# Optimization experiments

Hardware: AMD Instinct MI355X
Metric: run time of the kernel (lower is better)

## Reference

```python
import jax, jax.numpy as jnp
import numpy as np

N_NODES = 100000
N_EDGES = 1600000
C = 64          # in = hidden = out channels
L = 3           # num_layers
BN_EPS = 1e-5


def setup_inputs() -> dict:
    key = jax.random.key(0)
    ks = jax.random.split(key, 16)
    x = jax.random.normal(ks[0], (N_NODES, C), dtype=jnp.float32)
    edge_index = jax.random.randint(ks[1], (2, N_EDGES), 0, N_NODES, dtype=jnp.int32)
    s = 1.0 / np.sqrt(C)
    # Stacked per-layer parameters (all layers are C->C).
    # Linear weights stored as [in, out] (i.e. torch weight transposed).
    W1 = jax.random.normal(ks[2], (L, C, C), dtype=jnp.float32) * s
    b1 = jnp.zeros((L, C), dtype=jnp.float32)
    g1 = jnp.ones((L, C), dtype=jnp.float32)    # MLP BN1 gamma
    be1 = jnp.zeros((L, C), dtype=jnp.float32)  # MLP BN1 beta
    W2 = jax.random.normal(ks[3], (L, C, C), dtype=jnp.float32) * s
    b2 = jnp.zeros((L, C), dtype=jnp.float32)
    g2 = jnp.ones((L, C), dtype=jnp.float32)
    be2 = jnp.zeros((L, C), dtype=jnp.float32)
    bn_g = jnp.ones((L, C), dtype=jnp.float32)   # outer per-layer BN gamma
    bn_be = jnp.zeros((L, C), dtype=jnp.float32)
    eps = jnp.zeros((L,), dtype=jnp.float32)     # GIN eps per layer
    return {"x": x, "edge_index": edge_index, "eps": eps,
            "W1": W1, "b1": b1, "g1": g1, "be1": be1,
            "W2": W2, "b2": b2, "g2": g2, "be2": be2,
            "bn_g": bn_g, "bn_be": bn_be}


def _bn(h, g, b):
    # Inference-mode BatchNorm1d with running_mean=0, running_var=1.
    return g * (h * (1.0 / np.sqrt(1.0 + BN_EPS))) + b


def reference(x, edge_index, eps, W1, b1, g1, be1, W2, b2, g2, be2, bn_g, bn_be):
    src, dst = edge_index[0], edge_index[1]
    for i in range(L):
        # GIN message passing: gather source features, scatter-add to targets.
        agg = jax.ops.segment_sum(x[src], dst, num_segments=N_NODES)  # [N, C]
        h = (1.0 + eps[i]) * x + agg
        # 2-layer MLP: Linear -> BN -> ReLU, twice.
        h = jax.nn.relu(_bn(h @ W1[i] + b1[i], g1[i], be1[i]))
        h = jax.nn.relu(_bn(h @ W2[i] + b2[i], g2[i], be2[i]))
        # Outer per-layer BatchNorm.
        x = _bn(h, bn_g[i], bn_be[i])
        if i < L - 1:
            x = jax.nn.relu(x)  # dropout is identity in eval mode
    return x
```

## Files before the change

### kernel.cpp

```cpp
#include <hip/hip_runtime.h>
#include <hip/hip_fp16.h>

#define N_NODES 100000
#define N_EDGES 1600000
#define CH 64
#define NLAYERS 3
#define NBUCKC 98
#define SLABC 18432
#define SUBCAP 2304
#define EPB 8192

typedef _Float16 half8 __attribute__((ext_vector_type(8)));
typedef float floatx4 __attribute__((ext_vector_type(4)));

static __device__ __forceinline__ float4 ld4(const float* p){ return *(const float4*)p; }
static __device__ __forceinline__ unsigned pack2(float a, float b){
  __half2 h = __float22half2_rn(make_float2(a, b));
  return *(unsigned*)&h;
}
static __device__ __forceinline__ float2 up2(unsigned u){
  __half2 h = *(__half2*)&u;
  return __half22float2(h);
}

__global__ __launch_bounds__(256) void binit_kernel(int* __restrict__ btail){
  int i = blockIdx.x*256 + threadIdx.x;
  if (i < NBUCKC) btail[i] = i*SLABC;
}

__global__ __launch_bounds__(256) void part_kernel(const int* __restrict__ src, const int* __restrict__ dst,
                                                   int* __restrict__ btail, int* __restrict__ pairs){
  __shared__ int lpos[NBUCKC];
  __shared__ int gb[NBUCKC];
  int tid = threadIdx.x;
  if (tid < NBUCKC) lpos[tid] = 0;
  __syncthreads();
  int base = blockIdx.x * EPB;
  #pragma unroll 4
  for (int k = 0; k < EPB/256; ++k) {
    int e = base + k*256 + tid;
    if (e < N_EDGES) atomicAdd(&lpos[dst[e] >> 10], 1);
  }
  __syncthreads();
  if (tid < NBUCKC) {
    int cc = lpos[tid];
    gb[tid] = cc ? atomicAdd(&btail[tid], cc) : 0;
    lpos[tid] = 0;
  }
  __syncthreads();
  #pragma unroll 4
  for (int k = 0; k < EPB/256; ++k) {
    int e = base + k*256 + tid;
    if (e < N_EDGES) {
      int d = dst[e];
      int bk = d >> 10;
      int p = atomicAdd(&lpos[bk], 1);
      int idx = gb[bk] + p;
      if (idx < (bk+1)*SLABC)
        pairs[idx] = src[e] | ((d & 1023) << 20);
    }
  }
}

__global__ __launch_bounds__(256) void csr_kernel(const int* __restrict__ pairs, const int* __restrict__ btail,
                                                  int* __restrict__ offs, int* __restrict__ offe,
                                                  int* __restrict__ srclist){
  __shared__ int c[128];
  __shared__ int s[128];
  __shared__ int cur[128];
  int t = threadIdx.x;
  int b = blockIdx.x >> 3;
  int j = blockIdx.x & 7;
  int e0 = b*SLABC;
  int e1 = btail[b]; int emax = e0 + SLABC; if (e1 > emax) e1 = emax;
  if (t < 128) c[t] = 0;
  __syncthreads();
  for (int i = e0 + t; i < e1; i += 256) {
    int p = pairs[i];
    int dl = (unsigned)p >> 20;
    if ((dl >> 7) == j) atomicAdd(&c[dl & 127], 1);
  }
  __syncthreads();
  int v = (t < 128) ? c[t] : 0;
  if (t < 128) s[t] = v;
  __syncthreads();
  #pragma unroll
  for (int o = 1; o < 128; o <<= 1){
    int u = 0;
    if (t < 128 && t >= o) u = s[t-o];
    __syncthreads();
    if (t < 128) s[t] += u;
    __syncthreads();
  }
  int base = e0 + j*SUBCAP;
  if (t < 128) {
    int excl = s[t] - v;
    cur[t] = excl;
    int n = b*1024 + j*128 + t;
    if (n < N_NODES) { offs[n] = base + excl; offe[n] = base + excl + v; }
  }
  __syncthreads();
  for (int i = e0 + t; i < e1; i += 256) {
    int p = pairs[i];
    int dl = (unsigned)p >> 20;
    if ((dl >> 7) == j) {
      int pos = atomicAdd(&cur[dl & 127], 1);
      if (pos < SUBCAP)
        srclist[base + pos] = p & 0xFFFFF;
    }
  }
}

__global__ __launch_bounds__(256) void prep_kernel(
    const float* __restrict__ W1, const float* __restrict__ b1,
    const float* __restrict__ g1, const float* __restrict__ be1,
    const float* __restrict__ W2, const float* __restrict__ b2,
    const float* __restrict__ g2, const float* __restrict__ be2,
    const float* __restrict__ bng, const float* __restrict__ bnb,
    _Float16* __restrict__ Wt, float* __restrict__ bf, float* __restrict__ ogb){
  const float s = 0.9999950000374997f;
  int i = blockIdx.x*256 + threadIdx.x;
  if (i < NLAYERS*4096) {
    int l = i >> 12, rem = i & 4095, k = rem >> 6, n = rem & 63;
    int di = n*64 + (((k>>3) ^ (n&7))<<3) + (k&7);
    Wt[l*8192 + di]        = (_Float16)(W1[i] * g1[l*64+n] * s);
    Wt[l*8192 + 4096 + di] = (_Float16)(W2[i] * g2[l*64+n] * s);
  }
  if (i < NLAYERS*64) {
    int l = i >> 6, j = i & 63;
    bf[l*128 + j]      = b1[i]*g1[i]*s + be1[i];
    bf[l*128 + 64 + j] = b2[i]*g2[i]*s + be2[i];
    ogb[i]                 = bng[i]*s;
    ogb[NLAYERS*64 + i]    = bnb[i];
  }
}

__global__ __launch_bounds__(256) void xcvt_kernel(const float* __restrict__ x, unsigned short* __restrict__ xb){
  int i = (blockIdx.x*256 + threadIdx.x)*8;
  if (i < N_NODES*CH) {
    float4 v0 = ld4(x + i), v1 = ld4(x + i + 4);
    uint4 w;
    w.x = pack2(v0.x, v0.y); w.y = pack2(v0.z, v0.w);
    w.z = pack2(v1.x, v1.y); w.w = pack2(v1.z, v1.w);
    *(uint4*)(xb + i) = w;
  }
}

__global__ __launch_bounds__(256) void layer_kernel(const unsigned short* __restrict__ XBin,
                                                    const int* __restrict__ offs, const int* __restrict__ offe,
                                                    const int* __restrict__ srclist,
                                                    const float* __restrict__ eps,
                                                    const _Float16* __restrict__ Wt,
                                                    const float* __restrict__ bf, const float* __restrict__ ogb,
                                                    int layer, float* __restrict__ outf,
                                                    _Float16* __restrict__ outb, int relu_out){
  __shared__ _Float16 HsA[64*64];
  __shared__ _Float16 Wts[64*64];
  int tid = threadIdx.x;
  int b = blockIdx.x;
  const _Float16* Wg = Wt + layer*8192;
  *(uint4*)&Wts[tid*8]       = *(const uint4*)&Wg[tid*8];
  *(uint4*)&Wts[(tid+256)*8] = *(const uint4*)&Wg[(tid+256)*8];

  float ep = 1.0f + eps[layer];
  int kb = tid & 7;
  const unsigned short* xr = XBin + (kb << 3);
  #pragma unroll
  for (int p = 0; p < 2; ++p) {
    int nl = p*32 + (tid >> 3);
    int n = b*64 + nl;
    float A[8] = {0,0,0,0,0,0,0,0};
    float B[8] = {0,0,0,0,0,0,0,0};
    float C[8] = {0,0,0,0,0,0,0,0};
    float D[8] = {0,0,0,0,0,0,0,0};
    float r[8] = {0,0,0,0,0,0,0,0};
    if (n < N_NODES) {
      #define ADD8(acc, u) { float2 f; \
        f = up2((u).x); acc[0] += f.x; acc[1] += f.y; \
        f = up2((u).y); acc[2] += f.x; acc[3] += f.y; \
        f = up2((u).z); acc[4] += f.x; acc[5] += f.y; \
        f = up2((u).w); acc[6] += f.x; acc[7] += f.y; }
      int e0 = offs[n], e1 = offe[n];
      int e = e0;
      for (; e+4 <= e1; e += 4) {
        int s0 = srclist[e], s1 = srclist[e+1], s2 = srclist[e+2], s3 = srclist[e+3];
        uint4 u0 = *(const uint4*)(xr + (size_t)s0*CH);
        uint4 u1 = *(const uint4*)(xr + (size_t)s1*CH);
        uint4 u2 = *(const uint4*)(xr + (size_t)s2*CH);
        uint4 u3 = *(const uint4*)(xr + (size_t)s3*CH);
        ADD8(A, u0) ADD8(B, u1) ADD8(C, u2) ADD8(D, u3)
      }
      for (; e < e1; ++e) {
        int s0 = srclist[e];
        uint4 u0 = *(const uint4*)(xr + (size_t)s0*CH);
        ADD8(A, u0)
      }
      #undef ADD8
      uint4 sv = *(const uint4*)(xr + (size_t)n*CH);
      float sf[8];
      { float2 f;
        f = up2(sv.x); sf[0]=f.x; sf[1]=f.y;
        f = up2(sv.y); sf[2]=f.x; sf[3]=f.y;
        f = up2(sv.z); sf[4]=f.x; sf[5]=f.y;
        f = up2(sv.w); sf[6]=f.x; sf[7]=f.y; }
      #pragma unroll
      for (int i = 0; i < 8; ++i) r[i] = fmaf(ep, sf[i], (A[i] + B[i]) + (C[i] + D[i]));
    }
    uint4 w;
    w.x = pack2(r[0], r[1]); w.y = pack2(r[2], r[3]);
    w.z = pack2(r[4], r[5]); w.w = pack2(r[6], r[7]);
    *(uint4*)&HsA[nl*64 + ((kb ^ (nl&7))<<3)] = w;
  }
  __syncthreads();

  int lane = tid & 63;
  int wid = tid >> 6;
  int c = lane & 15;
  int q = lane >> 4;
  int mbase = wid*16;
  int ma = mbase + c;

  half8 a0 = *(const half8*)&HsA[ma*64 + (((q)   ^ (ma&7))<<3)];
  half8 a1 = *(const half8*)&HsA[ma*64 + (((4+q) ^ (ma&7))<<3)];

  floatx4 acc[4];
  #pragma unroll
  for (int nt = 0; nt < 4; ++nt) {
    int n = nt*16 + c;
    float bv = bf[layer*128 + n];
    floatx4 Acc = {bv, bv, bv, bv};
    half8 b0 = *(const half8*)&Wts[n*64 + (((q)   ^ (n&7))<<3)];
    half8 b1 = *(const half8*)&Wts[n*64 + (((4+q) ^ (n&7))<<3)];
    Acc = __builtin_amdgcn_mfma_f32_16x16x32_f16(a0, b0, Acc, 0, 0, 0);
    Acc = __builtin_amdgcn_mfma_f32_16x16x32_f16(a1, b1, Acc, 0, 0, 0);
    acc[nt] = Acc;
  }
  __syncthreads();

  #pragma unroll
  for (int nt = 0; nt < 4; ++nt) {
    int n = nt*16 + c;
    #pragma unroll
    for (int r = 0; r < 4; ++r) {
      int m = mbase + q*4 + r;
      float h = acc[nt][r]; h = h > 0.f ? h : 0.f;
      HsA[m*64 + (((n>>3) ^ (m&7))<<3) + (n&7)] = (_Float16)h;
    }
  }
  *(uint4*)&Wts[tid*8]       = *(const uint4*)&Wg[4096 + tid*8];
  *(uint4*)&Wts[(tid+256)*8] = *(const uint4*)&Wg[4096 + (tid+256)*8];
  __syncthreads();

  half8 c0 = *(const half8*)&HsA[ma*64 + (((q)   ^ (ma&7))<<3)];
  half8 c1 = *(const half8*)&HsA[ma*64 + (((4+q) ^ (ma&7))<<3)];
  floatx4 acc2[4];
  #pragma unroll
  for (int nt = 0; nt < 4; ++nt) {
    int n = nt*16 + c;
    float bv = bf[layer*128 + 64 + n];
    floatx4 Acc = {bv, bv, bv, bv};
    half8 b0 = *(const half8*)&Wts[n*64 + (((q)   ^ (n&7))<<3)];
    half8 b1 = *(const half8*)&Wts[n*64 + (((4+q) ^ (n&7))<<3)];
    Acc = __builtin_amdgcn_mfma_f32_16x16x32_f16(c0, b0, Acc, 0, 0, 0);
    Acc = __builtin_amdgcn_mfma_f32_16x16x32_f16(c1, b1, Acc, 0, 0, 0);
    acc2[nt] = Acc;
  }

  #pragma unroll
  for (int nt = 0; nt < 4; ++nt) {
    int n = nt*16 + c;
    float og = ogb[layer*64 + n];
    float ob = ogb[NLAYERS*64 + layer*64 + n];
    #pragma unroll
    for (int r = 0; r < 4; ++r) {
      int m = mbase + q*4 + r;
      int gnode = b*64 + m;
      if (gnode < N_NODES) {
        float h = acc2[nt][r]; h = h > 0.f ? h : 0.f;
        float o = fmaf(og, h, ob);
        if (relu_out) {
          o = o > 0.f ? o : 0.f;
          outb[(size_t)gnode*CH + n] = (_Float16)o;
        } else {
          outf[(size_t)gnode*CH + n] = o;
        }
      }
    }
  }
}

extern "C" void kernel_launch(void* const* d_in, const int* in_sizes, int n_in,
                              void* d_out, int out_size, void* d_ws, size_t ws_size,
                              hipStream_t stream) {
  const float* x0  = (const float*)d_in[0];
  const int*   ei  = (const int*)d_in[1];
  const float* eps = (const float*)d_in[2];
  const float* W1  = (const float*)d_in[3];
  const float* b1  = (const float*)d_in[4];
  const float* g1  = (const float*)d_in[5];
  const float* be1 = (const float*)d_in[6];
  const float* W2  = (const float*)d_in[7];
  const float* b2  = (const float*)d_in[8];
  const float* g2  = (const float*)d_in[9];
  const float* be2 = (const float*)d_in[10];
  const float* bng = (const float*)d_in[11];
  const float* bnb = (const float*)d_in[12];
  const int* src = ei;
  const int* dst = ei + N_EDGES;
  float* OUT = (float*)d_out;

  char* p = (char*)d_ws;
  auto carve = [&](size_t bytes)->char*{ char* r = p; p += (bytes + 255) & ~(size_t)255; return r; };
  int*   offs    = (int*)carve((size_t)N_NODES*sizeof(int));
  int*   offe    = (int*)carve((size_t)N_NODES*sizeof(int));
  int*   btail   = (int*)carve(NBUCKC*sizeof(int));
  int*   pairs   = (int*)carve((size_t)NBUCKC*SLABC*sizeof(int));
  int*   srclist = (int*)carve((size_t)NBUCKC*SLABC*sizeof(int));
  unsigned short* XB0 = (unsigned short*)carve((size_t)N_NODES*CH*2);
  unsigned short* XB1 = (unsigned short*)carve((size_t)N_NODES*CH*2);
  _Float16* Wt   = (_Float16*)carve((size_t)NLAYERS*2*4096*2);
  float* bfb     = (float*)carve((size_t)NLAYERS*2*64*sizeof(float));
  float* ogb     = (float*)carve((size_t)2*NLAYERS*64*sizeof(float));

  const int npart = (N_EDGES + EPB - 1)/EPB;
  binit_kernel<<<1, 256, 0, stream>>>(btail);
  part_kernel<<<npart, 256, 0, stream>>>(src, dst, btail, pairs);
  csr_kernel<<<NBUCKC*8, 256, 0, stream>>>(pairs, btail, offs, offe, srclist);
  prep_kernel<<<48, 256, 0, stream>>>(W1,b1,g1,be1,W2,b2,g2,be2,bng,bnb,Wt,bfb,ogb);
  xcvt_kernel<<<(N_NODES*CH/8 + 255)/256, 256, 0, stream>>>(x0, XB0);

  const int nlb = (N_NODES + 63)/64;
  layer_kernel<<<nlb, 256, 0, stream>>>(XB0, offs, offe, srclist, eps, Wt, bfb, ogb, 0, OUT, (_Float16*)XB1, 1);
  layer_kernel<<<nlb, 256, 0, stream>>>(XB1, offs, offe, srclist, eps, Wt, bfb, ogb, 1, OUT, (_Float16*)XB0, 1);
  layer_kernel<<<nlb, 256, 0, stream>>>(XB0, offs, offe, srclist, eps, Wt, bfb, ogb, 2, OUT, (_Float16*)XB1, 0);
}
```

Baseline: 322.2 us.

## Add second-level fine bucket partition before CSR build

```diff
diff --git a/kernel.cpp b/kernel.cpp
--- a/kernel.cpp
+++ b/kernel.cpp
@@ -7,7 +7,8 @@
 #define NLAYERS 3
 #define NBUCKC 98
 #define SLABC 18432
-#define SUBCAP 2304
+#define NFINE (NBUCKC*8)
+#define SLABF 2560
 #define EPB 8192
 
 typedef _Float16 half8 __attribute__((ext_vector_type(8)));
@@ -23,13 +24,14 @@
   return __half22float2(h);
 }
 
-__global__ __launch_bounds__(256) void binit_kernel(int* __restrict__ btail){
+__global__ __launch_bounds__(256) void binit_kernel(int* __restrict__ btail, int* __restrict__ ftail){
   int i = blockIdx.x*256 + threadIdx.x;
   if (i < NBUCKC) btail[i] = i*SLABC;
-}
-
-__global__ __launch_bounds__(256) void part_kernel(const int* __restrict__ src, const int* __restrict__ dst,
-                                                   int* __restrict__ btail, int* __restrict__ pairs){
+  if (i < NFINE)  ftail[i] = i*SLABF;
+}
+
+__global__ __launch_bounds__(256) void part1_kernel(const int* __restrict__ src, const int* __restrict__ dst,
+                                                    int* __restrict__ btail, int* __restrict__ pairs){
   __shared__ int lpos[NBUCKC];
   __shared__ int gb[NBUCKC];
   int tid = threadIdx.x;
@@ -62,23 +64,79 @@
   }
 }
 
-__global__ __launch_bounds__(256) void csr_kernel(const int* __restrict__ pairs, const int* __restrict__ btail,
+__global__ __launch_bounds__(256) void part2_kernel(const int* __restrict__ pairs, const int* __restrict__ btail,
+                                                    int* __restrict__ ftail, int* __restrict__ pairs2){
+  __shared__ int cnt[8*32];
+  __shared__ int scur[8];
+  int tid = threadIdx.x;
+  int b = blockIdx.x >> 3;
+  int sg = blockIdx.x & 7;
+  int e0 = b*SLABC;
+  int e1 = btail[b]; int emax = e0 + SLABC; if (e1 > emax) e1 = emax;
+  int len = e1 - e0;
+  int s0 = e0 + (int)(((long)len * sg) >> 3);
+  int s1 = e0 + (int)(((long)len * (sg+1)) >> 3);
+  if (tid < 256) { cnt[tid & 255] = 0; }
+  __syncthreads();
+  for (int i = s0 + tid; i < s1; i += 256) {
+    int p = pairs[i];
+    int fk = ((unsigned)p >> 27);
+    atomicAdd(&cnt[(fk<<5) + (tid & 31)], 1);
+  }
+  __syncthreads();
+  if (tid < 8) {
+    int tot = 0;
+    #pragma unroll
+    for (int r = 0; r < 32; ++r) tot += cnt[(tid<<5) + r];
+    scur[tid] = tot ? atomicAdd(&ftail[(b<<3) + tid], tot) : 0;
+  }
+  __syncthreads();
+  int lane = tid & 63;
+  int wbase = s0 + (tid >> 6)*64;
+  for (int i = wbase; i < s1; i += 256) {
+    int idx = i + lane - (tid >> 6)*64 + (tid >> 6)*64;
+    int e = i + lane - lane + lane;
+    (void)idx; (void)e;
+    int ei = i + lane - lane;
+    int my = ei + lane;
+    bool valid = (my < s1);
+    int p = valid ? pairs[my] : 0;
+    int fk = valid ? (int)((unsigned)p >> 27) : -1;
+    #pragma unroll
+    for (int j = 0; j < 8; ++j) {
+      unsigned long long mask = __ballot(valid && fk == j);
+      if (mask) {
+        int leader = __ffsll((long long)mask) - 1;
+        int cc = __popcll(mask);
+        int basep = 0;
+        if (lane == leader) basep = atomicAdd(&scur[j], cc);
+        basep = __shfl(basep, leader, 64);
+        if (valid && fk == j) {
+          int rank = __popcll(mask & ((1ull << lane) - 1ull));
+          int pos = basep + rank;
+          if (pos < ((b<<3) + j + 1)*SLABF)
+            pairs2[pos] = p;
+        }
+      }
+    }
+  }
+}
+
+__global__ __launch_bounds__(256) void csr_kernel(const int* __restrict__ pairs2, const int* __restrict__ ftail,
                                                   int* __restrict__ offs, int* __restrict__ offe,
                                                   int* __restrict__ srclist){
   __shared__ int c[128];
   __shared__ int s[128];
   __shared__ int cur[128];
   int t = threadIdx.x;
-  int b = blockIdx.x >> 3;
-  int j = blockIdx.x & 7;
-  int e0 = b*SLABC;
-  int e1 = btail[b]; int emax = e0 + SLABC; if (e1 > emax) e1 = emax;
+  int f = blockIdx.x;
+  int e0 = f*SLABF;
+  int e1 = ftail[f]; int emax = e0 + SLABF; if (e1 > emax) e1 = emax;
   if (t < 128) c[t] = 0;
   __syncthreads();
   for (int i = e0 + t; i < e1; i += 256) {
-    int p = pairs[i];
-    int dl = (unsigned)p >> 20;
-    if ((dl >> 7) == j) atomicAdd(&c[dl & 127], 1);
+    int p = pairs2[i];
+    atomicAdd(&c[((unsigned)p >> 20) & 127], 1);
   }
   __syncthreads();
   int v = (t < 128) ? c[t] : 0;
@@ -92,22 +150,18 @@
     if (t < 128) s[t] += u;
     __syncthreads();
   }
-  int base = e0 + j*SUBCAP;
   if (t < 128) {
     int excl = s[t] - v;
     cur[t] = excl;
-    int n = b*1024 + j*128 + t;
-    if (n < N_NODES) { offs[n] = base + excl; offe[n] = base + excl + v; }
+    int n = (f >> 3)*1024 + (f & 7)*128 + t;
+    if (n < N_NODES) { offs[n] = e0 + excl; offe[n] = e0 + excl + v; }
   }
   __syncthreads();
   for (int i = e0 + t; i < e1; i += 256) {
-    int p = pairs[i];
-    int dl = (unsigned)p >> 20;
-    if ((dl >> 7) == j) {
-      int pos = atomicAdd(&cur[dl & 127], 1);
-      if (pos < SUBCAP)
-        srclist[base + pos] = p & 0xFFFFF;
-    }
+    int p = pairs2[i];
+    int pos = atomicAdd(&cur[((unsigned)p >> 20) & 127], 1);
+    if (pos < SLABF)
+      srclist[e0 + pos] = p & 0xFFFFF;
   }
 }
 
@@ -314,8 +368,10 @@
   int*   offs    = (int*)carve((size_t)N_NODES*sizeof(int));
   int*   offe    = (int*)carve((size_t)N_NODES*sizeof(int));
   int*   btail   = (int*)carve(NBUCKC*sizeof(int));
+  int*   ftail   = (int*)carve(NFINE*sizeof(int));
   int*   pairs   = (int*)carve((size_t)NBUCKC*SLABC*sizeof(int));
-  int*   srclist = (int*)carve((size_t)NBUCKC*SLABC*sizeof(int));
+  int*   pairs2  = (int*)carve((size_t)NFINE*SLABF*sizeof(int));
+  int*   srclist = (int*)carve((size_t)NFINE*SLABF*sizeof(int));
   unsigned short* XB0 = (unsigned short*)carve((size_t)N_NODES*CH*2);
   unsigned short* XB1 = (unsigned short*)carve((size_t)N_NODES*CH*2);
   _Float16* Wt   = (_Float16*)carve((size_t)NLAYERS*2*4096*2);
@@ -323,9 +379,10 @@
   float* ogb     = (float*)carve((size_t)2*NLAYERS*64*sizeof(float));
 
   const int npart = (N_EDGES + EPB - 1)/EPB;
-  binit_kernel<<<1, 256, 0, stream>>>(btail);
-  part_kernel<<<npart, 256, 0, stream>>>(src, dst, btail, pairs);
-  csr_kernel<<<NBUCKC*8, 256, 0, stream>>>(pairs, btail, offs, offe, srclist);
+  binit_kernel<<<(NFINE+255)/256, 256, 0, stream>>>(btail, ftail);
+  part1_kernel<<<npart, 256, 0, stream>>>(src, dst, btail, pairs);
+  part2_kernel<<<NFINE, 256, 0, stream>>>(pairs, btail, ftail, pairs2);
+  csr_kernel<<<NFINE, 256, 0, stream>>>(pairs2, ftail, offs, offe, srclist);
   prep_kernel<<<48, 256, 0, stream>>>(W1,b1,g1,be1,W2,b2,g2,be2,bng,bnb,Wt,bfb,ogb);
   xcvt_kernel<<<(N_NODES*CH/8 + 255)/256, 256, 0, stream>>>(x0, XB0);
 
```

Measured after the change: 306.9 us. 1.05x faster.
